# Performance work log

Measured on AMD Instinct MI355X. Metric: run time of the kernel, lower is better.

## Reference

```python
import jax, jax.numpy as jnp
import numpy as np
from jax import lax

EPS = 1e-5
SLOPE = 0.01  # LeakyReLU negative slope
MAX_DISP = 5
KSIZE = 3  # correlation patch kernel size


def conv_bn_lrelu(x, w, b, g, be, stride=1):
    # x: (B, Cin, L), w: (Cout, Cin, K)
    k = w.shape[-1]
    pad = (k - 1) // 2
    y = lax.conv_general_dilated(x, w, (stride,), [(pad, pad)],
                                 dimension_numbers=('NCH', 'OIH', 'NCH'))
    y = y + b[None, :, None]
    # BatchNorm1d in training mode: biased batch stats over (B, L)
    m = y.mean(axis=(0, 2), keepdims=True)
    v = y.var(axis=(0, 2), keepdims=True)
    y = g[None, :, None] * (y - m) * lax.rsqrt(v + EPS) + be[None, :, None]
    return jnp.where(y >= 0, y, SLOPE * y)


def upsample_nearest(x, size):
    # F.interpolate(mode='nearest'): idx = floor(i * L_in / L_out)
    L = x.shape[-1]
    idx = (jnp.arange(size) * L) // size
    return x[:, :, idx]


def fusion(f1, f2, K=KSIZE, D=MAX_DISP):
    # Banded correlation: corr[b, d, i] = <patch1[b,:,i], patch2[b,:,clamp(i+d)]>
    # where patches stack K clamped neighbors along the channel dim.
    B, C, N = f1.shape
    h = K // 2
    win = jnp.clip(jnp.arange(N)[:, None] + jnp.arange(-h, h + 1)[None, :], 0, N - 1)  # (N, K)
    p1 = f1[:, :, win].transpose(0, 1, 3, 2).reshape(B, C * K, N)
    p2 = f2[:, :, win].transpose(0, 1, 3, 2).reshape(B, C * K, N)
    pts = jnp.arange(N)
    bands = []
    for d in range(-D, D + 1):  # small fixed loop over 2D+1 = 11 displacements
        j = jnp.clip(pts + d, 0, N - 1)
        bands.append(jnp.sum(p1 * p2[:, :, j], axis=1))  # (B, N)
    return jnp.stack(bands, axis=1)  # (B, 2D+1, N)


def _make_block(key, cin, cout, k):
    kw, _ = jax.random.split(key)
    scale = np.sqrt(2.0 / (1.0 + 0.1 ** 2) / (cin * k)).astype(np.float32)
    w = jax.random.normal(kw, (cout, cin, k), dtype=jnp.float32) * scale
    b = jnp.zeros((cout,), jnp.float32)
    g = jnp.ones((cout,), jnp.float32)
    be = jnp.zeros((cout,), jnp.float32)
    return w, b, g, be


def setup_inputs() -> dict:
    key = jax.random.key(0)
    ks = jax.random.split(key, 8)
    B, N, CIN = 8, 16384, 1
    scan1 = jax.random.normal(ks[0], (B, N, CIN), dtype=jnp.float32)
    inp = {'scan1': scan1}
    specs = [('enc0', CIN, 64, 3), ('enc1', 64, 128, 3), ('enc2', 128, 256, 3),
             ('dec1', 2 * MAX_DISP + 1 + 128, 128, 3), ('dec0', 128 + 64, 128, 3),
             ('flow', 128 + CIN, 2, 1)]
    for i, (name, cin, cout, k) in enumerate(specs):
        w, b, g, be = _make_block(ks[i + 1], cin, cout, k)
        inp[name + '_w'] = w
        inp[name + '_b'] = b
        inp[name + '_g'] = g
        inp[name + '_be'] = be
    return inp


def reference(scan1,
              enc0_w, enc0_b, enc0_g, enc0_be,
              enc1_w, enc1_b, enc1_g, enc1_be,
              enc2_w, enc2_b, enc2_g, enc2_be,
              dec1_w, dec1_b, dec1_g, dec1_be,
              dec0_w, dec0_b, dec0_g, dec0_be,
              flow_w, flow_b, flow_g, flow_be):
    x1 = scan1.transpose(0, 2, 1)  # (B, Cin, N)
    # scan2 defaults to scan1, so feat2_* == feat1_* (identical BN batch stats)
    f0 = conv_bn_lrelu(x1, enc0_w, enc0_b, enc0_g, enc0_be, stride=2)
    f1 = conv_bn_lrelu(f0, enc1_w, enc1_b, enc1_g, enc1_be, stride=2)
    f2 = conv_bn_lrelu(f1, enc2_w, enc2_b, enc2_g, enc2_be, stride=2)
    feat = fusion(f2, f2)  # (B, 11, N/8)
    up1 = upsample_nearest(feat, f1.shape[-1])
    up1 = jnp.concatenate((f1, up1), axis=1)
    up1 = conv_bn_lrelu(up1, dec1_w, dec1_b, dec1_g, dec1_be, stride=1)
    up0 = upsample_nearest(up1, f0.shape[-1])
    up0 = jnp.concatenate((f0, up0), axis=1)
    up0 = conv_bn_lrelu(up0, dec0_w, dec0_b, dec0_g, dec0_be, stride=1)
    out = upsample_nearest(up0, x1.shape[-1])
    out = jnp.concatenate((x1, out), axis=1)
    out = conv_bn_lrelu(out, flow_w, flow_b, flow_g, flow_be, stride=1)
    return out.transpose(0, 2, 1)  # (B, N, 2)
```

## Files before the change

kernel.cpp:

```cpp
#include <hip/hip_runtime.h>
#include <cstddef>

#define SLOPE 0.01f
#define BN_EPS 1e-5f

typedef __attribute__((ext_vector_type(8))) short short8;
typedef __attribute__((ext_vector_type(4))) float floatx4;

__device__ __forceinline__ float lrelu(float t) { return fmaxf(t, SLOPE * t); }

__device__ __forceinline__ unsigned short f2bf(float f) {
    union { float f; unsigned int u; } x; x.f = f;
    unsigned int r = (x.u + 0x7fff + ((x.u >> 16) & 1)) >> 16;
    return (unsigned short)r;
}
__device__ __forceinline__ float bf2f(unsigned short h) {
    union { unsigned int u; float f; } x; x.u = ((unsigned int)h) << 16;
    return x.f;
}

__device__ __forceinline__ void bn_coeff(const float* __restrict__ st,
                                         const float* __restrict__ g,
                                         const float* __restrict__ be,
                                         float invN, int c, float& sc, float& sh) {
    float m   = st[c] * invN;
    float var = fmaf(st[256 + c], invN, -m * m);
    float r   = rsqrtf(var + BN_EPS);
    sc = g[c] * r;
    sh = fmaf(-sc, m, be[c]);
}

__global__ __launch_bounds__(256) void prepw_kernel(
    const float* __restrict__ w, unsigned short* __restrict__ wr,
    int Cout, int Cinpad, int Cin)
{
    int id = blockIdx.x * 256 + threadIdx.x;
    if (id >= 3 * Cout * Cinpad) return;
    int ci = id % Cinpad;
    int rest = id / Cinpad;
    int co = rest % Cout;
    int t  = rest / Cout;
    float v = (ci < Cin) ? w[((size_t)co * Cin + ci) * 3 + t] : 0.0f;
    wr[id] = f2bf(v);
}

__global__ __launch_bounds__(256) void enc0_kernel(
    const float* __restrict__ x, const float* __restrict__ w,
    const float* __restrict__ bias, unsigned short* __restrict__ f0,
    float* __restrict__ st)
{
    __shared__ float ssum[64], ssq[64];
    const int tid = threadIdx.x;
    const int co  = tid & 63;
    const int b   = blockIdx.z;
    if (tid < 64) { ssum[tid] = 0.f; ssq[tid] = 0.f; }
    __syncthreads();
    const float w0 = w[co * 3], w1 = w[co * 3 + 1], w2 = w[co * 3 + 2];
    const float bs = bias[co];
    const float* xb = x + (size_t)b * 16384;
    float lsum = 0.f, lsq = 0.f;
    const int obase = blockIdx.x * 128 + (tid >> 6) * 32;
    for (int k = 0; k < 32; ++k) {
        int o = obase + k;
        int xi = 2 * o - 1;
        float x0v = (xi >= 0) ? xb[xi] : 0.f;
        float a = bs;
        a = fmaf(w0, x0v, a);
        a = fmaf(w1, xb[xi + 1], a);
        a = fmaf(w2, xb[xi + 2], a);
        f0[((size_t)(b * 8192 + o)) * 64 + co] = f2bf(a);
        lsum += a; lsq = fmaf(a, a, lsq);
    }
    atomicAdd(&ssum[co], lsum);
    atomicAdd(&ssq[co], lsq);
    __syncthreads();
    if (tid < 64) {
        atomicAdd(&st[tid],       ssum[tid]);
        atomicAdd(&st[256 + tid], ssq[tid]);
    }
}

template<int STRIDE>
__global__ __launch_bounds__(256) void conv_mfma_kernel(
    const unsigned short* __restrict__ xA, int CAc,
    const unsigned short* __restrict__ xB, int CBc,
    const unsigned short* __restrict__ Wr, const float* __restrict__ bias,
    unsigned short* __restrict__ out, int L_in, int L_out, int Cout,
    float* __restrict__ st)
{
    constexpr int SEG = 255 * STRIDE + 3;
    __shared__ __align__(16) unsigned short x_tile[SEG * 32];
    __shared__ __align__(16) unsigned short w_tile[3 * 64 * 32];
    __shared__ float ssum[64], ssq[64];

    const int tid  = threadIdx.x;
    const int wv   = tid >> 6;
    const int lane = tid & 63;
    const int col  = lane & 15;
    const int quad = lane >> 4;
    const int oblk = blockIdx.x * 256;
    const int cob  = blockIdx.y * 64;
    const int b    = blockIdx.z;
    const int nch    = CAc + CBc;
    const int CApad  = CAc * 32;
    const int CBpad  = CBc * 32;
    const int Cinpad = nch * 32;
    const int LB     = L_in >> 1;

    if (tid < 64) { ssum[tid] = 0.f; ssq[tid] = 0.f; }

    floatx4 acc[4][4];
    #pragma unroll
    for (int ps = 0; ps < 4; ++ps)
        #pragma unroll
        for (int s = 0; s < 4; ++s)
            acc[ps][s] = (floatx4){0.f, 0.f, 0.f, 0.f};

    const int x0 = oblk * STRIDE - 1;

    for (int ch = 0; ch < nch; ++ch) {
        __syncthreads();
        for (int r = tid; r < SEG * 4; r += 256) {
            const int pi = r >> 2, part = r & 3;
            const int gp = x0 + pi;
            short8 v = {0, 0, 0, 0, 0, 0, 0, 0};
            if (gp >= 0 && gp < L_in) {
                if (ch < CAc)
                    v = *(const short8*)(xA + ((size_t)b * L_in + gp) * CApad + ch * 32 + part * 8);
                else
                    v = *(const short8*)(xB + ((size_t)b * LB + (gp >> 1)) * CBpad + (ch - CAc) * 32 + part * 8);
            }
            *(short8*)(x_tile + pi * 32 + part * 8) = v;
        }
        for (int r = tid; r < 768; r += 256) {
            const int part = r & 3;
            const int co   = (r >> 2) & 63;
            const int t    = r >> 8;
            short8 v = *(const short8*)(Wr + ((size_t)t * Cout + cob + co) * Cinpad + ch * 32 + part * 8);
            *(short8*)(w_tile + (t * 64 + co) * 32 + part * 8) = v;
        }
        __syncthreads();
        #pragma unroll
        for (int t = 0; t < 3; ++t) {
            short8 bfr[4];
            #pragma unroll
            for (int s = 0; s < 4; ++s)
                bfr[s] = *(const short8*)(w_tile + (t * 64 + s * 16 + col) * 32 + quad * 8);
            #pragma unroll
            for (int ps = 0; ps < 4; ++ps) {
                const int xi = (wv * 64 + ps * 16 + col) * STRIDE + t;
                short8 afr = *(const short8*)(x_tile + xi * 32 + quad * 8);
                #pragma unroll
                for (int s = 0; s < 4; ++s)
                    acc[ps][s] = __builtin_amdgcn_mfma_f32_16x16x32_bf16(afr, bfr[s], acc[ps][s], 0, 0, 0);
            }
        }
    }

    float bv[4];
    #pragma unroll
    for (int s = 0; s < 4; ++s) bv[s] = bias[cob + s * 16 + col];
    #pragma unroll
    for (int ps = 0; ps < 4; ++ps)
        #pragma unroll
        for (int s = 0; s < 4; ++s)
            #pragma unroll
            for (int r = 0; r < 4; ++r)
                acc[ps][s][r] += bv[s];

    #pragma unroll
    for (int ps = 0; ps < 4; ++ps) {
        const int pos0 = oblk + wv * 64 + ps * 16 + quad * 4;
        #pragma unroll
        for (int s = 0; s < 4; ++s) {
            unsigned short* op = out + ((size_t)b * L_out + pos0) * Cout + cob + s * 16 + col;
            #pragma unroll
            for (int r = 0; r < 4; ++r)
                op[(size_t)r * Cout] = f2bf(acc[ps][s][r]);
        }
    }

    #pragma unroll
    for (int s = 0; s < 4; ++s) {
        float v = 0.f, q = 0.f;
        #pragma unroll
        for (int ps = 0; ps < 4; ++ps)
            #pragma unroll
            for (int r = 0; r < 4; ++r) {
                float a = acc[ps][s][r];
                v += a; q = fmaf(a, a, q);
            }
        v += __shfl_xor(v, 16); v += __shfl_xor(v, 32);
        q += __shfl_xor(q, 16); q += __shfl_xor(q, 32);
        if (quad == 0) {
            atomicAdd(&ssum[s * 16 + col], v);
            atomicAdd(&ssq[s * 16 + col],  q);
        }
    }
    __syncthreads();
    if (tid < 64) {
        atomicAdd(&st[cob + tid],       ssum[tid]);
        atomicAdd(&st[256 + cob + tid], ssq[tid]);
    }
}

__global__ __launch_bounds__(256) void bn_kernel(
    unsigned short* __restrict__ y, const float* __restrict__ st,
    const float* __restrict__ g, const float* __restrict__ be,
    float invN, int C, int n8)
{
    __shared__ float lsc[256], lsh[256];
    const int tid = threadIdx.x;
    if (tid < C) {
        float sc, sh;
        bn_coeff(st, g, be, invN, tid, sc, sh);
        lsc[tid] = sc; lsh[tid] = sh;
    }
    __syncthreads();
    int idx = blockIdx.x * 256 + tid;
    if (idx < n8) {
        short8 v = *(short8*)(y + (size_t)idx * 8);
        int c0 = (idx * 8) & (C - 1);
        #pragma unroll
        for (int j = 0; j < 8; ++j) {
            float f = bf2f((unsigned short)v[j]);
            f = lrelu(fmaf(f, lsc[c0 + j], lsh[c0 + j]));
            v[j] = (short)f2bf(f);
        }
        *(short8*)(y + (size_t)idx * 8) = v;
    }
}

__global__ __launch_bounds__(256) void fusion_kernel(
    const unsigned short* __restrict__ f2, unsigned short* __restrict__ feat)
{
    constexpr int ROWS = 76;
    constexpr int CPAD = 272;
    __shared__ __align__(16) unsigned short tile[ROWS * CPAD];
    const int tid = threadIdx.x;
    const int p0  = blockIdx.x * 64;
    const int b   = blockIdx.y;
    const unsigned short* base = f2 + (size_t)b * 2048 * 256;

    for (int r = tid; r < ROWS * 32; r += 256) {
        int row = r >> 5, piece = r & 31;
        int grow = min(max(p0 - 6 + row, 0), 2047);
        short8 v = *(const short8*)(base + (size_t)grow * 256 + piece * 8);
        *(short8*)(tile + row * CPAD + piece * 8) = v;
    }
    __syncthreads();

    const int il = tid >> 2;
    const int q  = tid & 3;
    const int i  = p0 + il;

    float acc[11];
    #pragma unroll
    for (int d = 0; d < 11; ++d) acc[d] = 0.f;

    int ra[3];
    #pragma unroll
    for (int j = 0; j < 3; ++j)
        ra[j] = (min(max(i + j - 1, 0), 2047) - p0 + 6) * CPAD;
    int rb[11][3];
    #pragma unroll
    for (int d = 0; d < 11; ++d) {
        int i2 = min(max(i + d - 5, 0), 2047);
        #pragma unroll
        for (int j = 0; j < 3; ++j)
            rb[d][j] = (min(max(i2 + j - 1, 0), 2047) - p0 + 6) * CPAD;
    }

    for (int ck = 0; ck < 8; ++ck) {
        const int coff = q * 64 + ck * 8;
        float fa[3][8];
        #pragma unroll
        for (int j = 0; j < 3; ++j) {
            short8 v = *(const short8*)(tile + ra[j] + coff);
            #pragma unroll
            for (int e = 0; e < 8; ++e) fa[j][e] = bf2f((unsigned short)v[e]);
        }
        #pragma unroll
        for (int d = 0; d < 11; ++d) {
            #pragma unroll
            for (int j = 0; j < 3; ++j) {
                short8 v = *(const short8*)(tile + rb[d][j] + coff);
                #pragma unroll
                for (int e = 0; e < 8; ++e)
                    acc[d] = fmaf(fa[j][e], bf2f((unsigned short)v[e]), acc[d]);
            }
        }
    }

    #pragma unroll
    for (int d = 0; d < 11; ++d) {
        acc[d] += __shfl_xor(acc[d], 1);
        acc[d] += __shfl_xor(acc[d], 2);
    }
    if (q == 0) {
        unsigned short* op = feat + ((size_t)(b * 2048 + i)) * 32;
        #pragma unroll
        for (int d = 0; d < 11; ++d) op[d] = f2bf(acc[d]);
        #pragma unroll
        for (int d = 11; d < 32; ++d) op[d] = 0;
    }
}

__global__ __launch_bounds__(256) void flow_kernel(
    const float* __restrict__ scan1, const unsigned short* __restrict__ d0,
    const float* __restrict__ fw, const float* __restrict__ fb,
    float* __restrict__ outr, float* __restrict__ st)
{
    __shared__ float s4[4][4];
    const int tid = threadIdx.x;
    const int b = blockIdx.z;
    const int i = blockIdx.x * 256 + tid;
    float sv = scan1[(size_t)b * 16384 + i];
    const unsigned short* row = d0 + ((size_t)(b * 8192 + (i >> 1))) * 128;
    float a0 = fmaf(fw[0],   sv, fb[0]);
    float a1 = fmaf(fw[129], sv, fb[1]);
    for (int c8 = 0; c8 < 16; ++c8) {
        short8 v = *(const short8*)(row + c8 * 8);
        #pragma unroll
        for (int j = 0; j < 8; ++j) {
            float f = bf2f((unsigned short)v[j]);
            int cc = c8 * 8 + j;
            a0 = fmaf(fw[1 + cc],   f, a0);
            a1 = fmaf(fw[130 + cc], f, a1);
        }
    }
    float2 o; o.x = a0; o.y = a1;
    *(float2*)(outr + ((size_t)(b * 16384 + i)) * 2) = o;
    float s0 = a0, q0 = a0 * a0, s1 = a1, q1 = a1 * a1;
    #pragma unroll
    for (int off = 1; off < 64; off <<= 1) {
        s0 += __shfl_xor(s0, off); q0 += __shfl_xor(q0, off);
        s1 += __shfl_xor(s1, off); q1 += __shfl_xor(q1, off);
    }
    if ((tid & 63) == 0) {
        int w = tid >> 6;
        s4[w][0] = s0; s4[w][1] = q0; s4[w][2] = s1; s4[w][3] = q1;
    }
    __syncthreads();
    if (tid == 0) {
        float t0 = 0, t1 = 0, t2 = 0, t3 = 0;
        for (int w = 0; w < 4; ++w) {
            t0 += s4[w][0]; t1 += s4[w][1]; t2 += s4[w][2]; t3 += s4[w][3];
        }
        atomicAdd(&st[0],   t0); atomicAdd(&st[256],     t1);
        atomicAdd(&st[1],   t2); atomicAdd(&st[256 + 1], t3);
    }
}

__global__ __launch_bounds__(256) void final_kernel(
    const float* __restrict__ raw, const float* __restrict__ st,
    const float* __restrict__ g, const float* __restrict__ be,
    float invN, float* __restrict__ out)
{
    int idx = blockIdx.x * 256 + threadIdx.x;
    float sc0, sh0, sc1, sh1;
    bn_coeff(st, g, be, invN, 0, sc0, sh0);
    bn_coeff(st, g, be, invN, 1, sc1, sh1);
    float2 v = *(const float2*)(raw + (size_t)idx * 2);
    float2 o;
    o.x = lrelu(fmaf(v.x, sc0, sh0));
    o.y = lrelu(fmaf(v.y, sc1, sh1));
    *(float2*)(out + (size_t)idx * 2) = o;
}


extern "C" void kernel_launch(void* const* d_in, const int* in_sizes, int n_in,
                              void* d_out, int out_size, void* d_ws, size_t ws_size,
                              hipStream_t stream)
{
    const int B = 8;
    const float* scan1 = (const float*)d_in[0];
    const float* enc0_w = (const float*)d_in[1];
    const float* enc0_b = (const float*)d_in[2];
    const float* enc0_g = (const float*)d_in[3];
    const float* enc0_be= (const float*)d_in[4];
    const float* enc1_w = (const float*)d_in[5];
    const float* enc1_b = (const float*)d_in[6];
    const float* enc1_g = (const float*)d_in[7];
    const float* enc1_be= (const float*)d_in[8];
    const float* enc2_w = (const float*)d_in[9];
    const float* enc2_b = (const float*)d_in[10];
    const float* enc2_g = (const float*)d_in[11];
    const float* enc2_be= (const float*)d_in[12];
    const float* dec1_w = (const float*)d_in[13];
    const float* dec1_b = (const float*)d_in[14];
    const float* dec1_g = (const float*)d_in[15];
    const float* dec1_be= (const float*)d_in[16];
    const float* dec0_w = (const float*)d_in[17];
    const float* dec0_b = (const float*)d_in[18];
    const float* dec0_g = (const float*)d_in[19];
    const float* dec0_be= (const float*)d_in[20];
    const float* flow_w = (const float*)d_in[21];
    const float* flow_b = (const float*)d_in[22];
    const float* flow_g = (const float*)d_in[23];
    const float* flow_be= (const float*)d_in[24];

    char* ws = (char*)d_ws;
    unsigned short* f0    = (unsigned short*)(ws);
    unsigned short* f1    = (unsigned short*)(ws + 8388608);
    unsigned short* f2    = (unsigned short*)(ws + 16777216);
    unsigned short* featn = (unsigned short*)(ws + 25165824);
    unsigned short* d1    = (unsigned short*)(ws + 26214400);
    unsigned short* d0    = (unsigned short*)(ws + 34603008);
    float*  flow_r = (float*)(ws + 51380224);
    unsigned short* wr1 = (unsigned short*)(ws + 52428800);
    unsigned short* wr2 = (unsigned short*)(ws + 52477952);
    unsigned short* wr3 = (unsigned short*)(ws + 52674560);
    unsigned short* wr4 = (unsigned short*)(ws + 52797440);
    float* st = (float*)(ws + 52944896);
    float* st0 = st, *st1 = st + 512, *st2 = st + 1024;
    float* st3 = st + 1536, *st4 = st + 2048, *st5 = st + 2560;

    const float iN0 = 1.0f / (B * 8192.0f);
    const float iN1 = 1.0f / (B * 4096.0f);
    const float iN2 = 1.0f / (B * 2048.0f);
    const float iN3 = 1.0f / (B * 4096.0f);
    const float iN4 = 1.0f / (B * 8192.0f);
    const float iN5 = 1.0f / (B * 16384.0f);

    hipMemsetAsync(st, 0, 6 * 512 * sizeof(float), stream);

    prepw_kernel<<<(3 * 128 * 64  + 255) / 256, 256, 0, stream>>>(enc1_w, wr1, 128, 64, 64);
    prepw_kernel<<<(3 * 256 * 128 + 255) / 256, 256, 0, stream>>>(enc2_w, wr2, 256, 128, 128);
    prepw_kernel<<<(3 * 128 * 160 + 255) / 256, 256, 0, stream>>>(dec1_w, wr3, 128, 160, 139);
    prepw_kernel<<<(3 * 128 * 192 + 255) / 256, 256, 0, stream>>>(dec0_w, wr4, 128, 192, 192);

    enc0_kernel<<<dim3(64, 1, B), 256, 0, stream>>>(scan1, enc0_w, enc0_b, f0, st0);
    bn_kernel<<<2048, 256, 0, stream>>>(f0, st0, enc0_g, enc0_be, iN0, 64, 524288);

    conv_mfma_kernel<2><<<dim3(16, 2, B), 256, 0, stream>>>(
        f0, 2, nullptr, 0, wr1, enc1_b, f1, 8192, 4096, 128, st1);
    bn_kernel<<<2048, 256, 0, stream>>>(f1, st1, enc1_g, enc1_be, iN1, 128, 524288);

    conv_mfma_kernel<2><<<dim3(8, 4, B), 256, 0, stream>>>(
        f1, 4, nullptr, 0, wr2, enc2_b, f2, 4096, 2048, 256, st2);
    bn_kernel<<<2048, 256, 0, stream>>>(f2, st2, enc2_g, enc2_be, iN2, 256, 524288);

    fusion_kernel<<<dim3(32, B), 256, 0, stream>>>(f2, featn);

    conv_mfma_kernel<1><<<dim3(16, 2, B), 256, 0, stream>>>(
        f1, 4, featn, 1, wr3, dec1_b, d1, 4096, 4096, 128, st3);
    bn_kernel<<<2048, 256, 0, stream>>>(d1, st3, dec1_g, dec1_be, iN3, 128, 524288);

    conv_mfma_kernel<1><<<dim3(32, 2, B), 256, 0, stream>>>(
        f0, 2, d1, 4, wr4, dec0_b, d0, 8192, 8192, 128, st4);
    bn_kernel<<<4096, 256, 0, stream>>>(d0, st4, dec0_g, dec0_be, iN4, 128, 1048576);

    flow_kernel<<<dim3(64, 1, B), 256, 0, stream>>>(scan1, d0, flow_w, flow_b, flow_r, st5);
    final_kernel<<<512, 256, 0, stream>>>(flow_r, st5, flow_g, flow_be, iN5, (float*)d_out);
}
```

Measured before the change: 280.4 us.

## Fuse BatchNorm+LeakyReLU into consumer kernel loads and register-prefetch conv chunks

Removes the five standalone bn_kernel passes. Each consumer (conv, fusion, flow) now computes the BN scale and shift from the accumulated statistics and applies normalize plus LeakyReLU as it loads the raw pre-BN bf16 activations. The conv kernel also prefetches the next channel chunk into registers while computing the current one, and the four weight-prep launches are merged into one. This saves several full read-write passes over the activations and some launches, at the cost of recomputing the activation on every tile load, including halo reloads and the reuse of f0/f1 in the decoder, plus higher register pressure.

```diff
diff --git a/kernel.cpp b/kernel.cpp
--- a/kernel.cpp
+++ b/kernel.cpp
@@ -30,18 +30,35 @@
     sh = fmaf(-sc, m, be[c]);
 }
 
-__global__ __launch_bounds__(256) void prepw_kernel(
-    const float* __restrict__ w, unsigned short* __restrict__ wr,
-    int Cout, int Cinpad, int Cin)
-{
-    int id = blockIdx.x * 256 + threadIdx.x;
-    if (id >= 3 * Cout * Cinpad) return;
+__device__ __forceinline__ void reorder1(const float* __restrict__ w,
+                                         unsigned short* __restrict__ wr,
+                                         int Cout, int Cinpad, int Cin, int id) {
     int ci = id % Cinpad;
     int rest = id / Cinpad;
     int co = rest % Cout;
     int t  = rest / Cout;
     float v = (ci < Cin) ? w[((size_t)co * Cin + ci) * 3 + t] : 0.0f;
     wr[id] = f2bf(v);
+}
+
+__global__ __launch_bounds__(256) void prepw_all_kernel(
+    const float* __restrict__ w1, unsigned short* __restrict__ o1,
+    const float* __restrict__ w2, unsigned short* __restrict__ o2,
+    const float* __restrict__ w3, unsigned short* __restrict__ o3,
+    const float* __restrict__ w4, unsigned short* __restrict__ o4)
+{
+    int id = blockIdx.x * 256 + threadIdx.x;
+    const int n1 = 3 * 128 * 64;
+    const int n2 = 3 * 256 * 128;
+    const int n3 = 3 * 128 * 160;
+    const int n4 = 3 * 128 * 192;
+    if (id < n1) { reorder1(w1, o1, 128, 64, 64, id); return; }
+    id -= n1;
+    if (id < n2) { reorder1(w2, o2, 256, 128, 128, id); return; }
+    id -= n2;
+    if (id < n3) { reorder1(w3, o3, 128, 160, 139, id); return; }
+    id -= n3;
+    if (id < n4) { reorder1(w4, o4, 128, 192, 192, id); return; }
 }
 
 __global__ __launch_bounds__(256) void enc0_kernel(
@@ -83,15 +100,21 @@
 template<int STRIDE>
 __global__ __launch_bounds__(256) void conv_mfma_kernel(
     const unsigned short* __restrict__ xA, int CAc,
+    const float* __restrict__ stA, const float* __restrict__ gA,
+    const float* __restrict__ beA, float invNA,
     const unsigned short* __restrict__ xB, int CBc,
+    const float* __restrict__ stB, const float* __restrict__ gB,
+    const float* __restrict__ beB, float invNB,
     const unsigned short* __restrict__ Wr, const float* __restrict__ bias,
     unsigned short* __restrict__ out, int L_in, int L_out, int Cout,
     float* __restrict__ st)
 {
     constexpr int SEG = 255 * STRIDE + 3;
+    constexpr int XPC = (SEG * 4 + 255) / 256;
     __shared__ __align__(16) unsigned short x_tile[SEG * 32];
     __shared__ __align__(16) unsigned short w_tile[3 * 64 * 32];
     __shared__ float ssum[64], ssq[64];
+    __shared__ float csc[192], csh[192];
 
     const int tid  = threadIdx.x;
     const int wv   = tid >> 6;
@@ -106,8 +129,16 @@
     const int CBpad  = CBc * 32;
     const int Cinpad = nch * 32;
     const int LB     = L_in >> 1;
+    const bool nA = (stA != nullptr);
+    const bool nB = (stB != nullptr);
 
     if (tid < 64) { ssum[tid] = 0.f; ssq[tid] = 0.f; }
+    for (int c = tid; c < Cinpad; c += 256) {
+        float sc = 1.f, sh = 0.f;
+        if (c < CApad) { if (nA) bn_coeff(stA, gA, beA, invNA, c, sc, sh); }
+        else           { if (nB) bn_coeff(stB, gB, beB, invNB, c - CApad, sc, sh); }
+        csc[c] = sc; csh[c] = sh;
+    }
 
     floatx4 acc[4][4];
     #pragma unroll
@@ -118,9 +149,11 @@
 
     const int x0 = oblk * STRIDE - 1;
 
-    for (int ch = 0; ch < nch; ++ch) {
-        __syncthreads();
-        for (int r = tid; r < SEG * 4; r += 256) {
+    short8 xr[XPC];
+    short8 wreg[3];
+    auto load_chunk = [&](int ch) {
+        int k = 0;
+        for (int r = tid; r < SEG * 4; r += 256, ++k) {
             const int pi = r >> 2, part = r & 3;
             const int gp = x0 + pi;
             short8 v = {0, 0, 0, 0, 0, 0, 0, 0};
@@ -130,16 +163,51 @@
                 else
                     v = *(const short8*)(xB + ((size_t)b * LB + (gp >> 1)) * CBpad + (ch - CAc) * 32 + part * 8);
             }
-            *(short8*)(x_tile + pi * 32 + part * 8) = v;
-        }
-        for (int r = tid; r < 768; r += 256) {
+            xr[k] = v;
+        }
+        int k2 = 0;
+        for (int r = tid; r < 768; r += 256, ++k2) {
             const int part = r & 3;
             const int co   = (r >> 2) & 63;
             const int t    = r >> 8;
-            short8 v = *(const short8*)(Wr + ((size_t)t * Cout + cob + co) * Cinpad + ch * 32 + part * 8);
-            *(short8*)(w_tile + (t * 64 + co) * 32 + part * 8) = v;
+            wreg[k2] = *(const short8*)(Wr + ((size_t)t * Cout + cob + co) * Cinpad + ch * 32 + part * 8);
+        }
+    };
+
+    load_chunk(0);
+    __syncthreads();
+
+    for (int ch = 0; ch < nch; ++ch) {
+        const bool applyN = (ch < CAc) ? nA : nB;
+        if (applyN) {
+            const int cb = ch * 32 + (tid & 3) * 8;
+            float scr[8], shr[8];
+            #pragma unroll
+            for (int e = 0; e < 8; ++e) { scr[e] = csc[cb + e]; shr[e] = csh[cb + e]; }
+            int k = 0;
+            for (int r = tid; r < SEG * 4; r += 256, ++k) {
+                const int gp = x0 + (r >> 2);
+                if (gp < 0 || gp >= L_in) continue;
+                #pragma unroll
+                for (int e = 0; e < 8; ++e) {
+                    float f = bf2f((unsigned short)xr[k][e]);
+                    f = lrelu(fmaf(f, scr[e], shr[e]));
+                    xr[k][e] = (short)f2bf(f);
+                }
+            }
         }
         __syncthreads();
+        {
+            int k = 0;
+            for (int r = tid; r < SEG * 4; r += 256, ++k)
+                *(short8*)(x_tile + (size_t)r * 8) = xr[k];
+            int k2 = 0;
+            for (int r = tid; r < 768; r += 256, ++k2)
+                *(short8*)(w_tile + (size_t)r * 8) = wreg[k2];
+        }
+        __syncthreads();
+        if (ch + 1 < nch) load_chunk(ch + 1);
+
         #pragma unroll
         for (int t = 0; t < 3; ++t) {
             short8 bfr[4];
@@ -204,48 +272,43 @@
     }
 }
 
-__global__ __launch_bounds__(256) void bn_kernel(
-    unsigned short* __restrict__ y, const float* __restrict__ st,
-    const float* __restrict__ g, const float* __restrict__ be,
-    float invN, int C, int n8)
-{
-    __shared__ float lsc[256], lsh[256];
-    const int tid = threadIdx.x;
-    if (tid < C) {
-        float sc, sh;
-        bn_coeff(st, g, be, invN, tid, sc, sh);
-        lsc[tid] = sc; lsh[tid] = sh;
-    }
-    __syncthreads();
-    int idx = blockIdx.x * 256 + tid;
-    if (idx < n8) {
-        short8 v = *(short8*)(y + (size_t)idx * 8);
-        int c0 = (idx * 8) & (C - 1);
-        #pragma unroll
-        for (int j = 0; j < 8; ++j) {
-            float f = bf2f((unsigned short)v[j]);
-            f = lrelu(fmaf(f, lsc[c0 + j], lsh[c0 + j]));
-            v[j] = (short)f2bf(f);
-        }
-        *(short8*)(y + (size_t)idx * 8) = v;
-    }
-}
-
 __global__ __launch_bounds__(256) void fusion_kernel(
-    const unsigned short* __restrict__ f2, unsigned short* __restrict__ feat)
+    const unsigned short* __restrict__ f2,
+    const float* __restrict__ st, const float* __restrict__ g,
+    const float* __restrict__ be, float invN,
+    unsigned short* __restrict__ feat)
 {
     constexpr int ROWS = 76;
     constexpr int CPAD = 272;
     __shared__ __align__(16) unsigned short tile[ROWS * CPAD];
+    __shared__ float csc[256], csh[256];
     const int tid = threadIdx.x;
     const int p0  = blockIdx.x * 64;
     const int b   = blockIdx.y;
     const unsigned short* base = f2 + (size_t)b * 2048 * 256;
 
+    {
+        float sc, sh;
+        bn_coeff(st, g, be, invN, tid, sc, sh);
+        csc[tid] = sc; csh[tid] = sh;
+    }
+    __syncthreads();
+    float scr[8], shr[8];
+    {
+        const int cb = (tid & 31) * 8;
+        #pragma unroll
+        for (int e = 0; e < 8; ++e) { scr[e] = csc[cb + e]; shr[e] = csh[cb + e]; }
+    }
     for (int r = tid; r < ROWS * 32; r += 256) {
         int row = r >> 5, piece = r & 31;
         int grow = min(max(p0 - 6 + row, 0), 2047);
         short8 v = *(const short8*)(base + (size_t)grow * 256 + piece * 8);
+        #pragma unroll
+        for (int e = 0; e < 8; ++e) {
+            float f = bf2f((unsigned short)v[e]);
+            f = lrelu(fmaf(f, scr[e], shr[e]));
+            v[e] = (short)f2bf(f);
+        }
         *(short8*)(tile + row * CPAD + piece * 8) = v;
     }
     __syncthreads();
@@ -308,13 +371,22 @@
 
 __global__ __launch_bounds__(256) void flow_kernel(
     const float* __restrict__ scan1, const unsigned short* __restrict__ d0,
+    const float* __restrict__ st4, const float* __restrict__ g4,
+    const float* __restrict__ be4, float invN4,
     const float* __restrict__ fw, const float* __restrict__ fb,
     float* __restrict__ outr, float* __restrict__ st)
 {
     __shared__ float s4[4][4];
+    __shared__ float csc[128], csh[128];
     const int tid = threadIdx.x;
     const int b = blockIdx.z;
     const int i = blockIdx.x * 256 + tid;
+    if (tid < 128) {
+        float sc, sh;
+        bn_coeff(st4, g4, be4, invN4, tid, sc, sh);
+        csc[tid] = sc; csh[tid] = sh;
+    }
+    __syncthreads();
     float sv = scan1[(size_t)b * 16384 + i];
     const unsigned short* row = d0 + ((size_t)(b * 8192 + (i >> 1))) * 128;
     float a0 = fmaf(fw[0],   sv, fb[0]);
@@ -323,8 +395,9 @@
         short8 v = *(const short8*)(row + c8 * 8);
         #pragma unroll
         for (int j = 0; j < 8; ++j) {
+            int cc = c8 * 8 + j;
             float f = bf2f((unsigned short)v[j]);
-            int cc = c8 * 8 + j;
+            f = lrelu(fmaf(f, csc[cc], csh[cc]));
             a0 = fmaf(fw[1 + cc],   f, a0);
             a1 = fmaf(fw[130 + cc], f, a1);
         }
@@ -425,32 +498,35 @@
 
     hipMemsetAsync(st, 0, 6 * 512 * sizeof(float), stream);
 
-    prepw_kernel<<<(3 * 128 * 64  + 255) / 256, 256, 0, stream>>>(enc1_w, wr1, 128, 64, 64);
-    prepw_kernel<<<(3 * 256 * 128 + 255) / 256, 256, 0, stream>>>(enc2_w, wr2, 256, 128, 128);
-    prepw_kernel<<<(3 * 128 * 160 + 255) / 256, 256, 0, stream>>>(dec1_w, wr3, 128, 160, 139);
-    prepw_kernel<<<(3 * 128 * 192 + 255) / 256, 256, 0, stream>>>(dec0_w, wr4, 128, 192, 192);
+    prepw_all_kernel<<<1008, 256, 0, stream>>>(enc1_w, wr1, enc2_w, wr2,
+                                               dec1_w, wr3, dec0_w, wr4);
 
     enc0_kernel<<<dim3(64, 1, B), 256, 0, stream>>>(scan1, enc0_w, enc0_b, f0, st0);
-    bn_kernel<<<2048, 256, 0, stream>>>(f0, st0, enc0_g, enc0_be, iN0, 64, 524288);
 
     conv_mfma_kernel<2><<<dim3(16, 2, B), 256, 0, stream>>>(
-        f0, 2, nullptr, 0, wr1, enc1_b, f1, 8192, 4096, 128, st1);
-    bn_kernel<<<2048, 256, 0, stream>>>(f1, st1, enc1_g, enc1_be, iN1, 128, 524288);
+        f0, 2, st0, enc0_g, enc0_be, iN0,
+        nullptr, 0, nullptr, nullptr, nullptr, 0.f,
+        wr1, enc1_b, f1, 8192, 4096, 128, st1);
 
     conv_mfma_kernel<2><<<dim3(8, 4, B), 256, 0, stream>>>(
-        f1, 4, nullptr, 0, wr2, enc2_b, f2, 4096, 2048, 256, st2);
-    bn_kernel<<<2048, 256, 0, stream>>>(f2, st2, enc2_g, enc2_be, iN2, 256, 524288);
-
-    fusion_kernel<<<dim3(32, B), 256, 0, stream>>>(f2, featn);
+        f1, 4, st1, enc1_g, enc1_be, iN1,
+        nullptr, 0, nullptr, nullptr, nullptr, 0.f,
+        wr2, enc2_b, f2, 4096, 2048, 256, st2);
+
+    fusion_kernel<<<dim3(32, B), 256, 0, stream>>>(f2, st2, enc2_g, enc2_be, iN2, featn);
 
     conv_mfma_kernel<1><<<dim3(16, 2, B), 256, 0, stream>>>(
-        f1, 4, featn, 1, wr3, dec1_b, d1, 4096, 4096, 128, st3);
-    bn_kernel<<<2048, 256, 0, stream>>>(d1, st3, dec1_g, dec1_be, iN3, 128, 524288);
+        f1, 4, st1, enc1_g, enc1_be, iN1,
+        featn, 1, nullptr, nullptr, nullptr, 0.f,
+        wr3, dec1_b, d1, 4096, 4096, 128, st3);
 
     conv_mfma_kernel<1><<<dim3(32, 2, B), 256, 0, stream>>>(
-        f0, 2, d1, 4, wr4, dec0_b, d0, 8192, 8192, 128, st4);
-    bn_kernel<<<4096, 256, 0, stream>>>(d0, st4, dec0_g, dec0_be, iN4, 128, 1048576);
-
-    flow_kernel<<<dim3(64, 1, B), 256, 0, stream>>>(scan1, d0, flow_w, flow_b, flow_r, st5);
+        f0, 2, st0, enc0_g, enc0_be, iN0,
+        d1, 4, st3, dec1_g, dec1_be, iN3,
+        wr4, dec0_b, d0, 8192, 8192, 128, st4);
+
+    flow_kernel<<<dim3(64, 1, B), 256, 0, stream>>>(
+        scan1, d0, st4, dec0_g, dec0_be, iN4, flow_w, flow_b, flow_r, st5);
+
     final_kernel<<<512, 256, 0, stream>>>(flow_r, st5, flow_g, flow_be, iN5, (float*)d_out);
 }
```

New measurement: 993.9 us. +254.5%, slower.
